# Performance work log

Measured on AMD Instinct MI355X. Metric: run time of the kernel, lower is better.

The kernel has to match this reference:

```python
import jax, jax.numpy as jnp
import numpy as np

BS, M, CLIP_DIM = 64, 1000, 512
D = 512
N_WAYS = 20
N_Z = 8


def setup_inputs() -> dict:
    key = jax.random.key(0)
    ks = jax.random.split(key, 16)
    s = 0.02
    inp = {
        "x_context": jax.random.normal(ks[0], (BS, M, CLIP_DIM), jnp.float32),
        "y_context": jax.random.randint(ks[1], (BS, M), 0, N_WAYS),
        "x_query": jax.random.normal(ks[2], (BS, M, CLIP_DIM), jnp.float32),
        # image_proj
        "Wp": jax.random.normal(ks[3], (CLIP_DIM, D), jnp.float32) * s,
        "bp": jnp.zeros((D,), jnp.float32),
        # aggregator: Linear(d,d) -> GELU -> Linear(d,2d)
        "Wa1": jax.random.normal(ks[4], (D, D), jnp.float32) * s,
        "ba1": jnp.zeros((D,), jnp.float32),
        "Wa2": jax.random.normal(ks[5], (D, 2 * D), jnp.float32) * s,
        "ba2": jnp.zeros((2 * D,), jnp.float32),
        # decoder: Linear(d,d) -> GELU -> Linear(d,d)
        "Wd1": jax.random.normal(ks[6], (D, D), jnp.float32) * s,
        "bd1": jnp.zeros((D,), jnp.float32),
        "Wd2": jax.random.normal(ks[7], (D, D), jnp.float32) * s,
        "bd2": jnp.zeros((D,), jnp.float32),
    }
    return inp


def reference(x_context, y_context, x_query, Wp, bp, Wa1, ba1, Wa2, ba2, Wd1, bd1, Wd2, bd2):
    # project image embeddings: [bs, M, clip_dim] -> [bs, M, d]
    xc = x_context @ Wp + bp
    xq = x_query @ Wp + bp

    # encode_context_per_class: per-class masked sum == one-hot segment-sum
    # (original loops over classes doing (x*mask).sum(dim=1))
    oh = jax.nn.one_hot(y_context, N_WAYS, dtype=xc.dtype)  # [bs, M, N]
    r_C = jnp.einsum('bmn,bmd->bnd', oh, xc)  # [bs, N, d]

    # knowledge is None -> k = zeros; combined = relu(r + 0)
    combined = jax.nn.relu(r_C)
    h = jax.nn.gelu(combined @ Wa1 + ba1, approximate=False)
    stats = h @ Wa2 + ba2  # [bs, N, 2d]
    mu, scale_raw = stats[..., :D], stats[..., D:]
    scale = 0.01 + 0.99 * jax.nn.softplus(scale_raw)

    # eval path: sample n_z from q(z|C) via reparameterization
    eps = jax.random.normal(jax.random.key(42), (N_Z,) + mu.shape, mu.dtype)
    z_samples = mu[None] + scale[None] * eps  # [n_z, bs, N, d]

    # decode: class weight vectors then inner product with queries
    W = jax.nn.gelu(z_samples @ Wd1 + bd1, approximate=False) @ Wd2 + bd2
    logits = jnp.einsum('bqd,sbnd->sbqn', xq, W)  # [n_z, bs, Q*N, N]
    return logits, z_samples, mu, scale
```

## Files before the change

### kernel.cpp

```cpp
#include <hip/hip_runtime.h>
#include <hip/hip_bf16.h>
#include <stdint.h>


typedef __attribute__((ext_vector_type(8))) short short8;
typedef __attribute__((ext_vector_type(4))) float f32x4;

__device__ __forceinline__ float gelu_f(float x) {
    return 0.5f * x * (1.0f + erff(x * 0.70710678118654752440f));
}
__device__ __forceinline__ float softplus_f(float x) {
    return fmaxf(x, 0.0f) + log1pf(expf(-fabsf(x)));
}
__device__ __forceinline__ uint32_t cvt2(float a, float b) {
    __hip_bfloat162 h;
    h.x = __float2bfloat16(a);
    h.y = __float2bfloat16(b);
    uint32_t u; __builtin_memcpy(&u, &h, 4); return u;
}
__device__ __forceinline__ unsigned short f2bfu(float f) {
    __hip_bfloat16 h = __float2bfloat16(f);
    unsigned short u; __builtin_memcpy(&u, &h, 2); return u;
}
__device__ __forceinline__ float bfu2f(unsigned short u) {
    uint32_t v = (uint32_t)u << 16; float f; __builtin_memcpy(&f, &v, 4); return f;
}

__device__ __forceinline__ void threefry2x32(uint32_t k0, uint32_t k1,
                                             uint32_t x0, uint32_t x1,
                                             uint32_t& o0, uint32_t& o1) {
    uint32_t ks[3] = {k0, k1, k0 ^ k1 ^ 0x1BD11BDAu};
    x0 += ks[0]; x1 += ks[1];
    const uint32_t rot[8] = {13,15,26,6,17,29,16,24};
#pragma unroll
    for (int i = 0; i < 5; i++) {
#pragma unroll
        for (int j = 0; j < 4; j++) {
            uint32_t r = rot[(i & 1) * 4 + j];
            x0 += x1;
            x1 = (x1 << r) | (x1 >> (32 - r));
            x1 ^= x0;
        }
        x0 += ks[(i + 1) % 3];
        x1 += ks[(i + 2) % 3] + (uint32_t)(i + 1);
    }
    o0 = x0; o1 = x1;
}

__device__ __forceinline__ float bits_to_normal(uint32_t b) {
    float f = __uint_as_float((b >> 9) | 0x3F800000u) - 1.0f;
    const float lo = __uint_as_float(0xBF7FFFFFu);
    float u = fmaxf(lo, f * 2.0f + lo);
    return 1.41421356237309504880f * erfinvf(u);
}

__global__ __launch_bounds__(256) void prep_k(
    const float* __restrict__ Wp, const float* __restrict__ Wa1,
    const float* __restrict__ Wa2, const float* __restrict__ Wd1,
    const float* __restrict__ Wd2, const float* __restrict__ bp,
    const float* __restrict__ bd2, const int* __restrict__ y,
    unsigned short* __restrict__ WpTb, unsigned short* __restrict__ Wa1Tb,
    unsigned short* __restrict__ Wa2Tb, unsigned short* __restrict__ WdT1b,
    unsigned short* __restrict__ Gtb,
    float* __restrict__ bv, float* __restrict__ w2bp,
    float* __restrict__ c0, float* __restrict__ cnt)
{
    __shared__ __align__(16) char sm[24576];
    __shared__ int lc[32];
    __shared__ float ws4[4];
    const int f = blockIdx.x;
    const int tid = threadIdx.x;

    if (f < 320) {
        float (*T)[65] = reinterpret_cast<float(*)[65]>(sm);
        const float* src; unsigned short* dst; int C, t, xb, yb;
        if (f < 64)       { src = Wp;  dst = WpTb;  C = 512;  t = f;       xb = t & 7;  yb = t >> 3; }
        else if (f < 128) { src = Wa1; dst = Wa1Tb; C = 512;  t = f - 64;  xb = t & 7;  yb = t >> 3; }
        else if (f < 256) { src = Wa2; dst = Wa2Tb; C = 1024; t = f - 128; xb = t & 15; yb = t >> 4; }
        else              { src = Wd1; dst = WdT1b; C = 512;  t = f - 256; xb = t & 7;  yb = t >> 3; }
        const int r0 = yb * 64, cc0 = xb * 64;
        const int rr = tid >> 4, cc = (tid & 15) * 4;
#pragma unroll
        for (int l = 0; l < 4; l++) {
            int row = rr + l * 16;
            float4 v = *(const float4*)&src[(size_t)(r0 + row) * C + cc0 + cc];
            T[row][cc] = v.x; T[row][cc+1] = v.y; T[row][cc+2] = v.z; T[row][cc+3] = v.w;
        }
        __syncthreads();
#pragma unroll
        for (int l = 0; l < 4; l++) {
            int n = rr + l * 16;
            uint2 u;
            u.x = cvt2(T[cc][n], T[cc+1][n]);
            u.y = cvt2(T[cc+2][n], T[cc+3][n]);
            *(uint2*)&dst[(size_t)(cc0 + n) * 512 + r0 + cc] = u;
        }
    } else if (f < 576) {
        const float* W = (f < 448) ? Wp : Wd2;
        const float* v = (f < 448) ? bd2 : bp;
        float* o = (f < 448) ? bv : w2bp;
        int t = (f < 448) ? f - 320 : f - 448;
        int wave = tid >> 6, lane = tid & 63;
        int r = t * 4 + wave;
        const float* row = W + (size_t)r * 512 + lane * 8;
        float4 x0 = *(const float4*)row;
        float4 x1 = *(const float4*)(row + 4);
        float4 v0 = *(const float4*)&v[lane * 8];
        float4 v1 = *(const float4*)&v[lane * 8 + 4];
        float s = x0.x*v0.x + x0.y*v0.y + x0.z*v0.z + x0.w*v0.w
                + x1.x*v1.x + x1.y*v1.y + x1.z*v1.z + x1.w*v1.w;
#pragma unroll
        for (int off = 32; off > 0; off >>= 1) s += __shfl_down(s, off, 64);
        if (lane == 0) o[r] = s;
    } else if (f == 576) {
        float s = bp[tid] * bd2[tid] + bp[tid + 256] * bd2[tid + 256];
#pragma unroll
        for (int off = 32; off > 0; off >>= 1) s += __shfl_down(s, off, 64);
        int wave = tid >> 6, lane = tid & 63;
        if (lane == 0) ws4[wave] = s;
        __syncthreads();
        if (tid == 0) c0[0] = ws4[0] + ws4[1] + ws4[2] + ws4[3];
    } else if (f < 641) {
        int b = f - 577;
        if (tid < 32) lc[tid] = 0;
        __syncthreads();
        for (int m = tid; m < 1000; m += 256)
            atomicAdd(&lc[y[b * 1000 + m]], 1);
        __syncthreads();
        if (tid < 20) cnt[b * 20 + tid] = (float)lc[tid];
    } else {
        unsigned short* As = (unsigned short*)sm;
        unsigned short* Bs = (unsigned short*)(sm + 8192);
        const int g = f - 641;
        const int lane = tid & 63, w = tid >> 6;
        const int row0 = (g >> 2) * 64, col0 = (g & 3) * 128;
        f32x4 acc[4][2] = {};
        for (int k0 = 0; k0 < 512; k0 += 64) {
            {
                int row = tid >> 2, cs = (tid & 3) * 16;
                int swz = (row & 7) << 4;
                const float* src = Wp + (size_t)(row0 + row) * 512 + k0 + cs;
#pragma unroll
                for (int j = 0; j < 2; j++) {
                    float4 v0 = *(const float4*)(src + j * 8);
                    float4 v1 = *(const float4*)(src + j * 8 + 4);
                    uint4 u;
                    u.x = cvt2(v0.x, v0.y); u.y = cvt2(v0.z, v0.w);
                    u.z = cvt2(v1.x, v1.y); u.w = cvt2(v1.z, v1.w);
                    *(uint4*)((char*)As + row * 128 + (((cs + j * 8) * 2) ^ swz)) = u;
                }
            }
            {
                int row = tid >> 1, cs = (tid & 1) * 32;
                int swz = (row & 7) << 4;
                const float* src = Wd2 + (size_t)(col0 + row) * 512 + k0 + cs;
#pragma unroll
                for (int j = 0; j < 4; j++) {
                    float4 v0 = *(const float4*)(src + j * 8);
                    float4 v1 = *(const float4*)(src + j * 8 + 4);
                    uint4 u;
                    u.x = cvt2(v0.x, v0.y); u.y = cvt2(v0.z, v0.w);
                    u.z = cvt2(v1.x, v1.y); u.w = cvt2(v1.z, v1.w);
                    *(uint4*)((char*)Bs + row * 128 + (((cs + j * 8) * 2) ^ swz)) = u;
                }
            }
            __syncthreads();
#pragma unroll
            for (int ks = 0; ks < 2; ks++) {
                short8 a[4], bb[2];
#pragma unroll
                for (int mi = 0; mi < 4; mi++) {
                    int r = mi * 16 + (lane & 15);
                    a[mi] = *(const short8*)((const char*)As + r * 128 +
                              (((ks * 32 + (lane >> 4) * 8) * 2) ^ ((r & 7) << 4)));
                }
#pragma unroll
                for (int ni = 0; ni < 2; ni++) {
                    int n = w * 32 + ni * 16 + (lane & 15);
                    bb[ni] = *(const short8*)((const char*)Bs + n * 128 +
                              (((ks * 32 + (lane >> 4) * 8) * 2) ^ ((n & 7) << 4)));
                }
#pragma unroll
                for (int mi = 0; mi < 4; mi++)
#pragma unroll
                    for (int ni = 0; ni < 2; ni++)
                        acc[mi][ni] = __builtin_amdgcn_mfma_f32_16x16x32_bf16(a[mi], bb[ni], acc[mi][ni], 0, 0, 0);
            }
            __syncthreads();
        }
#pragma unroll
        for (int mi = 0; mi < 4; mi++)
#pragma unroll
            for (int ni = 0; ni < 2; ni++) {
                int c = col0 + w * 32 + ni * 16 + (lane & 15);
#pragma unroll
                for (int j = 0; j < 4; j++) {
                    int r = row0 + mi * 16 + (lane >> 4) * 4 + j;
                    Gtb[(size_t)r * 512 + c] = f2bfu(acc[mi][ni][j]);
                }
            }
    }
}

__global__ __launch_bounds__(256) void onehot4_k(const float* __restrict__ xc,
                                                 const int* __restrict__ y,
                                                 float* __restrict__ Apart) {
    __shared__ unsigned short Xs[128 * 64];
    __shared__ int ys[256];
    const int chb = blockIdx.x * 128;
    const int mc = blockIdx.y;
    const int b = blockIdx.z;
    const int m00 = mc * 256;
    const int tid = threadIdx.x, lane = tid & 63, w = tid >> 6;
    const int chs = w * 32;

    {
        int mg = m00 + tid;
        ys[tid] = (mg < 1000) ? y[b * 1000 + mg] : -1;
    }

    f32x4 acc[2][2] = {};
    for (int step = 0; step < 4; step++) {
        const int k0 = step * 64;
        int m = m00 + k0 + lane; if (m > 999) m = 999;
        const float* src = xc + ((size_t)b * 1000 + m) * 512 + chb + chs;
        float x[32];
#pragma unroll
        for (int j8 = 0; j8 < 8; j8++) {
            float4 v = *(const float4*)(src + j8 * 4);
            x[j8*4+0]=v.x; x[j8*4+1]=v.y; x[j8*4+2]=v.z; x[j8*4+3]=v.w;
        }
        __syncthreads();
#pragma unroll
        for (int j = 0; j < 32; j++) {
            int ch = chs + j;
            *(unsigned short*)((char*)Xs + ch * 128 + ((lane * 2) ^ ((ch & 7) << 4)))
                = f2bfu(x[j]);
        }
        __syncthreads();
#pragma unroll
        for (int ks = 0; ks < 2; ks++) {
            int kb = ks * 32 + (lane >> 4) * 8;
            int4 yv0 = *(const int4*)&ys[k0 + kb];
            int4 yv1 = *(const int4*)&ys[k0 + kb + 4];
            int ya[8] = {yv0.x, yv0.y, yv0.z, yv0.w, yv1.x, yv1.y, yv1.z, yv1.w};
            short8 a[2];
#pragma unroll
            for (int mi = 0; mi < 2; mi++) {
                int cls = mi * 16 + (lane & 15);
#pragma unroll
                for (int e = 0; e < 8; e++)
                    a[mi][e] = (short)((ya[e] == cls) ? 0x3F80 : 0);
            }
            short8 bb[2];
#pragma unroll
            for (int ni = 0; ni < 2; ni++) {
                int ch = chs + ni * 16 + (lane & 15);
                bb[ni] = *(const short8*)((const char*)Xs + ch * 128 +
                           ((kb * 2) ^ ((ch & 7) << 4)));
            }
#pragma unroll
            for (int mi = 0; mi < 2; mi++)
#pragma unroll
                for (int ni = 0; ni < 2; ni++)
                    acc[mi][ni] = __builtin_amdgcn_mfma_f32_16x16x32_bf16(a[mi], bb[ni], acc[mi][ni], 0, 0, 0);
        }
    }
    float* dst = Apart + (size_t)mc * 655360;
#pragma unroll
    for (int mi = 0; mi < 2; mi++) {
#pragma unroll
        for (int ni = 0; ni < 2; ni++) {
            int ch = chb + chs + ni * 16 + (lane & 15);
#pragma unroll
            for (int j = 0; j < 4; j++) {
                int cls = mi * 16 + (lane >> 4) * 4 + j;
                if (cls < 20)
                    dst[((size_t)b * 20 + cls) * 512 + ch] = acc[mi][ni][j];
            }
        }
    }
}

template <int EPI, int MT, int A4>
__global__ __launch_bounds__(256) void gm2_k(const unsigned short* __restrict__ Abf,
                                             const unsigned short* __restrict__ Bbf,
                                             const float* __restrict__ bias,
                                             const float* __restrict__ extra,
                                             unsigned short* __restrict__ C0,
                                             float* __restrict__ F0,
                                             float* __restrict__ F1,
                                             int Nn) {
    __shared__ unsigned short As[MT * 64];
    __shared__ unsigned short Bs[128 * 64];
    const int tid = threadIdx.x;
    const int lane = tid & 63, w = tid >> 6;
    const int row0 = blockIdx.y * MT, col0 = blockIdx.x * 128;
    f32x4 acc[MT / 16][2] = {};
    for (int k0 = 0; k0 < 512; k0 += 64) {
        if constexpr (MT == 64) {
            int row = tid >> 2, cs = (tid & 3) * 16;
            int swz = (row & 7) << 4;
            const unsigned short* src = Abf + (size_t)(row0 + row) * 512 + k0 + cs;
#pragma unroll
            for (int j = 0; j < 2; j++) {
                uint4 u = *(const uint4*)(src + j * 8);
                *(uint4*)((char*)As + row * 128 + (((cs + j * 8) * 2) ^ swz)) = u;
            }
        } else {
            int row = tid >> 3, cs = (tid & 7) * 8;
            int swz = (row & 7) << 4;
            uint4 u;
            if constexpr (A4) {
                const float* p = (const float*)Abf + (size_t)(row0 + row) * 512 + k0 + cs;
                float4 s0 = *(const float4*)p;
                float4 s1 = *(const float4*)(p + 4);
#pragma unroll
                for (int q = 1; q < 4; q++) {
                    const float* pp = p + (size_t)q * 655360;
                    float4 v0 = *(const float4*)pp, v1 = *(const float4*)(pp + 4);
                    s0.x += v0.x; s0.y += v0.y; s0.z += v0.z; s0.w += v0.w;
                    s1.x += v1.x; s1.y += v1.y; s1.z += v1.z; s1.w += v1.w;
                }
                u.x = cvt2(s0.x, s0.y); u.y = cvt2(s0.z, s0.w);
                u.z = cvt2(s1.x, s1.y); u.w = cvt2(s1.z, s1.w);
            } else {
                u = *(const uint4*)(Abf + (size_t)(row0 + row) * 512 + k0 + cs);
            }
            *(uint4*)((char*)As + row * 128 + ((cs * 2) ^ swz)) = u;
        }
        {
            int row = tid >> 1, cs = (tid & 1) * 32;
            int swz = (row & 7) << 4;
            const unsigned short* src = Bbf + (size_t)(col0 + row) * 512 + k0 + cs;
#pragma unroll
            for (int j = 0; j < 4; j++) {
                uint4 u = *(const uint4*)(src + j * 8);
                *(uint4*)((char*)Bs + row * 128 + (((cs + j * 8) * 2) ^ swz)) = u;
            }
        }
        __syncthreads();
#pragma unroll
        for (int ks = 0; ks < 2; ks++) {
            short8 a[MT / 16], bb[2];
#pragma unroll
            for (int mi = 0; mi < MT / 16; mi++) {
                int r = mi * 16 + (lane & 15);
                a[mi] = *(const short8*)((const char*)As + r * 128 +
                          (((ks * 32 + (lane >> 4) * 8) * 2) ^ ((r & 7) << 4)));
            }
#pragma unroll
            for (int ni = 0; ni < 2; ni++) {
                int n = w * 32 + ni * 16 + (lane & 15);
                bb[ni] = *(const short8*)((const char*)Bs + n * 128 +
                          (((ks * 32 + (lane >> 4) * 8) * 2) ^ ((n & 7) << 4)));
            }
#pragma unroll
            for (int mi = 0; mi < MT / 16; mi++)
#pragma unroll
                for (int ni = 0; ni < 2; ni++)
                    acc[mi][ni] = __builtin_amdgcn_mfma_f32_16x16x32_bf16(a[mi], bb[ni], acc[mi][ni], 0, 0, 0);
        }
        __syncthreads();
    }
#pragma unroll
    for (int mi = 0; mi < MT / 16; mi++) {
#pragma unroll
        for (int ni = 0; ni < 2; ni++) {
            int c = col0 + w * 32 + ni * 16 + (lane & 15);
            float bvv = bias ? bias[c] : 0.f;
#pragma unroll
            for (int j = 0; j < 4; j++) {
                int r = row0 + mi * 16 + (lane >> 4) * 4 + j;
                float v = acc[mi][ni][j];
                if (EPI == 0) {
                    v += bvv;
                    C0[(size_t)r * Nn + c] = f2bfu(v);
                } else if (EPI == 1) {
                    v += extra[r] * bvv;
                    C0[(size_t)r * Nn + c] = f2bfu(fmaxf(v, 0.f));
                } else if (EPI == 2) {
                    C0[(size_t)r * Nn + c] = f2bfu(gelu_f(v + bvv));
                } else {
                    v += bvv;
                    if (c < 512) F0[(size_t)r * 512 + c] = v;
                    else F1[(size_t)r * 512 + (c - 512)] = 0.01f + 0.99f * softplus_f(v);
                }
            }
        }
    }
}

__global__ __launch_bounds__(256) void z2_k(const float* __restrict__ mu,
                                            const float* __restrict__ sc,
                                            float* __restrict__ z,
                                            unsigned short* __restrict__ zb) {
    const uint32_t NH = 2621440u;
    uint32_t i = blockIdx.x * 256u + threadIdx.x;
    if (i >= NH) return;
    uint32_t t0 = 2u * i;
    uint32_t o0, o1, p0, p1;
    threefry2x32(0u, 42u, 0u, t0, o0, o1);
    threefry2x32(0u, 42u, 0u, t0 + 1u, p0, p1);
    uint32_t r0 = t0 % 655360u;
    float2 mv = *(const float2*)&mu[r0];
    float2 sv = *(const float2*)&sc[r0];
    float z0 = mv.x + sv.x * bits_to_normal(o0 ^ o1);
    float z1 = mv.y + sv.y * bits_to_normal(p0 ^ p1);
    float2 zo; zo.x = z0; zo.y = z1;
    *(float2*)&z[t0] = zo;
    *(uint32_t*)&zb[t0] = cvt2(z0, z1);
}

__global__ __launch_bounds__(256) void beta2_k(const unsigned short* __restrict__ Wgb,
                                               const float* __restrict__ vec,
                                               const float* __restrict__ c0,
                                               float* __restrict__ beta) {
    int wave = threadIdx.x >> 6, lane = threadIdx.x & 63;
    int r = blockIdx.x * 4 + wave;
    short8 wv = *(const short8*)(Wgb + (size_t)r * 512 + lane * 8);
    float s = 0.f;
#pragma unroll
    for (int e = 0; e < 8; e++) s += vec[lane * 8 + e] * bfu2f((unsigned short)wv[e]);
#pragma unroll
    for (int o = 32; o > 0; o >>= 1) s += __shfl_down(s, o, 64);
    if (lane == 0) beta[r] = s + c0[0];
}

__global__ __launch_bounds__(512) void logits_mfma4_k(const float* __restrict__ Xq,
                                                      const unsigned short* __restrict__ Vb,
                                                      const float* __restrict__ beta,
                                                      float* __restrict__ out) {
    __shared__ unsigned short Vs[2][160 * 64];
    __shared__ float bs[160];
    const int u = blockIdx.x + 8 * blockIdx.y;
    const int xcd = u & 7, idx = u >> 3;
    const int b = (idx & 7) * 8 + xcd;
    const int qh = idx >> 3;
    const int tid = threadIdx.x, lane = tid & 63, w = tid >> 6;
    const int wq = w >> 1, wn = w & 1;

    if (tid < 160) {
        int s = tid / 20, n = tid - s * 20;
        bs[tid] = beta[(size_t)(s * 64 + b) * 20 + n];
    }

    auto stageV = [&](int buf, int k0) {
        for (int c = tid; c < 640; c += 512) {
            int row = c >> 2, off = (c & 3) * 32;
            int sdiv = row / 20;
            int row_g = row + sdiv * 1260 + b * 20;
            const unsigned short* src = Vb + (size_t)row_g * 512 + k0 + (c & 3) * 16;
            uint4 u0 = *(const uint4*)src;
            uint4 u1 = *(const uint4*)(src + 8);
            int swz = (row & 7) << 4;
            char* base = (char*)&Vs[buf][0] + row * 128;
            *(uint4*)(base + (off ^ swz)) = u0;
            *(uint4*)(base + ((off + 16) ^ swz)) = u1;
        }
    };

    const int klane = (lane >> 4) * 8;
    const float* xp[2];
    int qb[2];
#pragma unroll
    for (int qs = 0; qs < 2; qs++) {
        qb[qs] = qh * 128 + wq * 32 + qs * 16;
        int qr = qb[qs] + (lane & 15);
        if (qr > 999) qr = 999;
        xp[qs] = Xq + ((size_t)b * 1000 + qr) * 512 + klane;
    }
    int vrow[5], vswz[5];
#pragma unroll
    for (int nf = 0; nf < 5; nf++) {
        int rr = wn * 80 + nf * 16 + (lane & 15);
        vrow[nf] = rr * 128;
        vswz[nf] = (rr & 7) << 4;
    }

    stageV(0, 0);
    __syncthreads();

    f32x4 acc[2][5] = {};
    int cur = 0;
    for (int step = 0; step < 8; step++) {
        const int k0 = step * 64;
        if (step < 7) stageV(cur ^ 1, k0 + 64);
        const char* vbase = (const char*)&Vs[cur][0];
#pragma unroll
        for (int ks = 0; ks < 2; ks++) {
            int kb = (ks * 32 + klane) * 2;
            short8 bf[5];
#pragma unroll
            for (int nf = 0; nf < 5; nf++)
                bf[nf] = *(const short8*)(vbase + vrow[nf] + (kb ^ vswz[nf]));
            short8 af[2];
#pragma unroll
            for (int qs = 0; qs < 2; qs++) {
                const float* p = xp[qs] + k0 + ks * 32;
                float4 v0 = *(const float4*)p;
                float4 v1 = *(const float4*)(p + 4);
                uint4 uu;
                uu.x = cvt2(v0.x, v0.y); uu.y = cvt2(v0.z, v0.w);
                uu.z = cvt2(v1.x, v1.y); uu.w = cvt2(v1.z, v1.w);
                __builtin_memcpy(&af[qs], &uu, 16);
            }
#pragma unroll
            for (int qs = 0; qs < 2; qs++)
#pragma unroll
                for (int nf = 0; nf < 5; nf++)
                    acc[qs][nf] = __builtin_amdgcn_mfma_f32_16x16x32_bf16(af[qs], bf[nf], acc[qs][nf], 0, 0, 0);
        }
        __syncthreads();
        cur ^= 1;
    }

#pragma unroll
    for (int nf = 0; nf < 5; nf++) {
        int rl = wn * 80 + nf * 16 + (lane & 15);
        int s = rl / 20, n = rl - s * 20;
        float bb = bs[rl];
        size_t ob = (size_t)(s * 64 + b) * 20000;
#pragma unroll
        for (int qs = 0; qs < 2; qs++) {
#pragma unroll
            for (int j = 0; j < 4; j++) {
                int q = qb[qs] + (lane >> 4) * 4 + j;
                if (q < 1000)
                    out[ob + (size_t)q * 20 + n] = acc[qs][nf][j] + bb;
            }
        }
    }
}

extern "C" void kernel_launch(void* const* d_in, const int* in_sizes, int n_in,
                              void* d_out, int out_size, void* d_ws, size_t ws_size,
                              hipStream_t stream) {
    const float* x_context = (const float*)d_in[0];
    const int*   y_context = (const int*)d_in[1];
    const float* x_query   = (const float*)d_in[2];
    const float* Wp  = (const float*)d_in[3];
    const float* bp  = (const float*)d_in[4];
    const float* Wa1 = (const float*)d_in[5];
    const float* ba1 = (const float*)d_in[6];
    const float* Wa2 = (const float*)d_in[7];
    const float* ba2 = (const float*)d_in[8];
    const float* Wd1 = (const float*)d_in[9];
    const float* bd1 = (const float*)d_in[10];
    const float* Wd2 = (const float*)d_in[11];
    const float* bd2 = (const float*)d_in[12];

    float* out    = (float*)d_out;
    float* logits = out;
    float* z      = out + 10240000;
    float* mu     = out + 15482880;
    float* sc     = out + 16138240;

    float* ws   = (float*)d_ws;
    float* cnt  = ws;
    float* beta = cnt + 1280;
    float* bv   = beta + 10240;
    float* w2bp = bv + 512;
    float* c0   = w2bp + 512;
    unsigned short* WpTb  = (unsigned short*)(c0 + 63);
    unsigned short* Wa1Tb = WpTb + 262144;
    unsigned short* Wa2Tb = Wa1Tb + 262144;
    unsigned short* WdT1b = Wa2Tb + 524288;
    unsigned short* Gtb   = WdT1b + 262144;
    unsigned short* combb = Gtb + 262144;
    unsigned short* hb    = combb + 655360;
    unsigned short* zb    = hb + 655360;
    unsigned short* Vbf   = zb + 5242880;
    float* big = (float*)(Vbf + 5242880);
    unsigned short* Wgb = (unsigned short*)big;

    prep_k<<<dim3(673), 256, 0, stream>>>(Wp, Wa1, Wa2, Wd1, Wd2, bp, bd2, y_context,
                                          WpTb, Wa1Tb, Wa2Tb, WdT1b, Gtb,
                                          bv, w2bp, c0, cnt);
    onehot4_k<<<dim3(4, 4, 64), 256, 0, stream>>>(x_context, y_context, big);
    gm2_k<1, 32, 1><<<dim3(4, 40), 256, 0, stream>>>((const unsigned short*)big, WpTb, bp, cnt, combb, nullptr, nullptr, 512);
    gm2_k<2, 32, 0><<<dim3(4, 40), 256, 0, stream>>>(combb, Wa1Tb, ba1, nullptr, hb, nullptr, nullptr, 512);
    gm2_k<3, 32, 0><<<dim3(8, 40), 256, 0, stream>>>(hb, Wa2Tb, ba2, nullptr, nullptr, mu, sc, 1024);
    z2_k<<<dim3(10240), 256, 0, stream>>>(mu, sc, z, zb);
    gm2_k<2, 64, 0><<<dim3(4, 160), 256, 0, stream>>>(zb, WdT1b, bd1, nullptr, Wgb, nullptr, nullptr, 512);
    gm2_k<0, 64, 0><<<dim3(4, 160), 256, 0, stream>>>(Wgb, Gtb, bv, nullptr, Vbf, nullptr, nullptr, 512);
    beta2_k<<<dim3(2560), 256, 0, stream>>>(Wgb, w2bp, c0, beta);
    logits_mfma4_k<<<dim3(8, 64), 512, 0, stream>>>(x_query, Vbf, beta, logits);
}
```

Before: 224.2 us.

## Fuse onehot segment-sum into prep kernel and fuse decoder GEMMs with beta

The one-hot segment-sum blocks are appended to the weight-prep kernel as extra block indices, removing one launch. The two decoder GEMMs (z·Wd1 with GELU, then ·G) and the beta dot product become one kernel that keeps the 64x512 GELU intermediate in shared memory, so it is no longer written to or read back from global memory. The cost is that the fused kernel launches only 160 blocks of 512 threads with large shared memory, and its B operands come straight from global memory, so occupancy and parallelism drop compared with the earlier 640-block GEMMs.

```diff
diff --git a/kernel.cpp b/kernel.cpp
--- a/kernel.cpp
+++ b/kernel.cpp
@@ -54,19 +54,21 @@
     return 1.41421356237309504880f * erfinvf(u);
 }
 
-__global__ __launch_bounds__(256) void prep_k(
+__global__ __launch_bounds__(256) void po_k(
     const float* __restrict__ Wp, const float* __restrict__ Wa1,
     const float* __restrict__ Wa2, const float* __restrict__ Wd1,
     const float* __restrict__ Wd2, const float* __restrict__ bp,
     const float* __restrict__ bd2, const int* __restrict__ y,
+    const float* __restrict__ xc,
     unsigned short* __restrict__ WpTb, unsigned short* __restrict__ Wa1Tb,
     unsigned short* __restrict__ Wa2Tb, unsigned short* __restrict__ WdT1b,
     unsigned short* __restrict__ Gtb,
     float* __restrict__ bv, float* __restrict__ w2bp,
-    float* __restrict__ c0, float* __restrict__ cnt)
+    float* __restrict__ c0, float* __restrict__ cnt,
+    float* __restrict__ Apart)
 {
     __shared__ __align__(16) char sm[24576];
-    __shared__ int lc[32];
+    __shared__ int lc[256];
     __shared__ float ws4[4];
     const int f = blockIdx.x;
     const int tid = threadIdx.x;
@@ -128,7 +130,7 @@
             atomicAdd(&lc[y[b * 1000 + m]], 1);
         __syncthreads();
         if (tid < 20) cnt[b * 20 + tid] = (float)lc[tid];
-    } else {
+    } else if (f < 673) {
         unsigned short* As = (unsigned short*)sm;
         unsigned short* Bs = (unsigned short*)(sm + 8192);
         const int g = f - 641;
@@ -199,84 +201,79 @@
                     Gtb[(size_t)r * 512 + c] = f2bfu(acc[mi][ni][j]);
                 }
             }
-    }
-}
-
-__global__ __launch_bounds__(256) void onehot4_k(const float* __restrict__ xc,
-                                                 const int* __restrict__ y,
-                                                 float* __restrict__ Apart) {
-    __shared__ unsigned short Xs[128 * 64];
-    __shared__ int ys[256];
-    const int chb = blockIdx.x * 128;
-    const int mc = blockIdx.y;
-    const int b = blockIdx.z;
-    const int m00 = mc * 256;
-    const int tid = threadIdx.x, lane = tid & 63, w = tid >> 6;
-    const int chs = w * 32;
-
-    {
-        int mg = m00 + tid;
-        ys[tid] = (mg < 1000) ? y[b * 1000 + mg] : -1;
-    }
-
-    f32x4 acc[2][2] = {};
-    for (int step = 0; step < 4; step++) {
-        const int k0 = step * 64;
-        int m = m00 + k0 + lane; if (m > 999) m = 999;
-        const float* src = xc + ((size_t)b * 1000 + m) * 512 + chb + chs;
-        float x[32];
-#pragma unroll
-        for (int j8 = 0; j8 < 8; j8++) {
-            float4 v = *(const float4*)(src + j8 * 4);
-            x[j8*4+0]=v.x; x[j8*4+1]=v.y; x[j8*4+2]=v.z; x[j8*4+3]=v.w;
-        }
-        __syncthreads();
-#pragma unroll
-        for (int j = 0; j < 32; j++) {
-            int ch = chs + j;
-            *(unsigned short*)((char*)Xs + ch * 128 + ((lane * 2) ^ ((ch & 7) << 4)))
-                = f2bfu(x[j]);
-        }
-        __syncthreads();
-#pragma unroll
-        for (int ks = 0; ks < 2; ks++) {
-            int kb = ks * 32 + (lane >> 4) * 8;
-            int4 yv0 = *(const int4*)&ys[k0 + kb];
-            int4 yv1 = *(const int4*)&ys[k0 + kb + 4];
-            int ya[8] = {yv0.x, yv0.y, yv0.z, yv0.w, yv1.x, yv1.y, yv1.z, yv1.w};
-            short8 a[2];
-#pragma unroll
-            for (int mi = 0; mi < 2; mi++) {
-                int cls = mi * 16 + (lane & 15);
-#pragma unroll
-                for (int e = 0; e < 8; e++)
-                    a[mi][e] = (short)((ya[e] == cls) ? 0x3F80 : 0);
-            }
-            short8 bb[2];
+    } else {
+        unsigned short* Xs = (unsigned short*)sm;
+        int* ys = lc;
+        const int f2 = f - 673;
+        const int chb = (f2 & 3) * 128;
+        const int mc = (f2 >> 2) & 3;
+        const int b = f2 >> 4;
+        const int m00 = mc * 256;
+        const int lane = tid & 63, w = tid >> 6;
+        const int chs = w * 32;
+        {
+            int mg = m00 + tid;
+            ys[tid] = (mg < 1000) ? y[b * 1000 + mg] : -1;
+        }
+        f32x4 acc[2][2] = {};
+        for (int step = 0; step < 4; step++) {
+            const int k0 = step * 64;
+            int m = m00 + k0 + lane; if (m > 999) m = 999;
+            const float* src = xc + ((size_t)b * 1000 + m) * 512 + chb + chs;
+            float x[32];
+#pragma unroll
+            for (int j8 = 0; j8 < 8; j8++) {
+                float4 v = *(const float4*)(src + j8 * 4);
+                x[j8*4+0]=v.x; x[j8*4+1]=v.y; x[j8*4+2]=v.z; x[j8*4+3]=v.w;
+            }
+            __syncthreads();
+#pragma unroll
+            for (int j = 0; j < 32; j++) {
+                int ch = chs + j;
+                *(unsigned short*)((char*)Xs + ch * 128 + ((lane * 2) ^ ((ch & 7) << 4)))
+                    = f2bfu(x[j]);
+            }
+            __syncthreads();
+#pragma unroll
+            for (int ks = 0; ks < 2; ks++) {
+                int kb = ks * 32 + (lane >> 4) * 8;
+                int4 yv0 = *(const int4*)&ys[k0 + kb];
+                int4 yv1 = *(const int4*)&ys[k0 + kb + 4];
+                int ya[8] = {yv0.x, yv0.y, yv0.z, yv0.w, yv1.x, yv1.y, yv1.z, yv1.w};
+                short8 a[2];
+#pragma unroll
+                for (int mi = 0; mi < 2; mi++) {
+                    int cls = mi * 16 + (lane & 15);
+#pragma unroll
+                    for (int e = 0; e < 8; e++)
+                        a[mi][e] = (short)((ya[e] == cls) ? 0x3F80 : 0);
+                }
+                short8 bb[2];
+#pragma unroll
+                for (int ni = 0; ni < 2; ni++) {
+                    int ch = chs + ni * 16 + (lane & 15);
+                    bb[ni] = *(const short8*)((const char*)Xs + ch * 128 +
+                               ((kb * 2) ^ ((ch & 7) << 4)));
+                }
+#pragma unroll
+                for (int mi = 0; mi < 2; mi++)
+#pragma unroll
+                    for (int ni = 0; ni < 2; ni++)
+                        acc[mi][ni] = __builtin_amdgcn_mfma_f32_16x16x32_bf16(a[mi], bb[ni], acc[mi][ni], 0, 0, 0);
+            }
+        }
+        float* dst = Apart + (size_t)mc * 655360;
+#pragma unroll
+        for (int mi = 0; mi < 2; mi++) {
 #pragma unroll
             for (int ni = 0; ni < 2; ni++) {
-                int ch = chs + ni * 16 + (lane & 15);
-                bb[ni] = *(const short8*)((const char*)Xs + ch * 128 +
-                           ((kb * 2) ^ ((ch & 7) << 4)));
-            }
-#pragma unroll
-            for (int mi = 0; mi < 2; mi++)
-#pragma unroll
-                for (int ni = 0; ni < 2; ni++)
-                    acc[mi][ni] = __builtin_amdgcn_mfma_f32_16x16x32_bf16(a[mi], bb[ni], acc[mi][ni], 0, 0, 0);
-        }
-    }
-    float* dst = Apart + (size_t)mc * 655360;
-#pragma unroll
-    for (int mi = 0; mi < 2; mi++) {
-#pragma unroll
-        for (int ni = 0; ni < 2; ni++) {
-            int ch = chb + chs + ni * 16 + (lane & 15);
-#pragma unroll
-            for (int j = 0; j < 4; j++) {
-                int cls = mi * 16 + (lane >> 4) * 4 + j;
-                if (cls < 20)
-                    dst[((size_t)b * 20 + cls) * 512 + ch] = acc[mi][ni][j];
+                int ch = chb + chs + ni * 16 + (lane & 15);
+#pragma unroll
+                for (int j = 0; j < 4; j++) {
+                    int cls = mi * 16 + (lane >> 4) * 4 + j;
+                    if (cls < 20)
+                        dst[((size_t)b * 20 + cls) * 512 + ch] = acc[mi][ni][j];
+                }
             }
         }
     }
@@ -412,19 +409,122 @@
     *(uint32_t*)&zb[t0] = cvt2(z0, z1);
 }
 
-__global__ __launch_bounds__(256) void beta2_k(const unsigned short* __restrict__ Wgb,
-                                               const float* __restrict__ vec,
-                                               const float* __restrict__ c0,
-                                               float* __restrict__ beta) {
-    int wave = threadIdx.x >> 6, lane = threadIdx.x & 63;
-    int r = blockIdx.x * 4 + wave;
-    short8 wv = *(const short8*)(Wgb + (size_t)r * 512 + lane * 8);
-    float s = 0.f;
-#pragma unroll
-    for (int e = 0; e < 8; e++) s += vec[lane * 8 + e] * bfu2f((unsigned short)wv[e]);
-#pragma unroll
-    for (int o = 32; o > 0; o >>= 1) s += __shfl_down(s, o, 64);
-    if (lane == 0) beta[r] = s + c0[0];
+__global__ __launch_bounds__(512) void wgv_k(const unsigned short* __restrict__ zb,
+                                             const unsigned short* __restrict__ Wd1T,
+                                             const unsigned short* __restrict__ Gt,
+                                             const float* __restrict__ bd1,
+                                             const float* __restrict__ bv,
+                                             const float* __restrict__ w2bp,
+                                             const float* __restrict__ c0,
+                                             unsigned short* __restrict__ Vbf,
+                                             float* __restrict__ beta) {
+    __shared__ unsigned short Wg[64 * 512];
+    __shared__ unsigned short As[64 * 64];
+    const int r0 = blockIdx.x * 64;
+    const int tid = threadIdx.x, lane = tid & 63, w = tid >> 6;
+    const int col0 = w * 64;
+
+    f32x4 acc[4][4] = {};
+    for (int k0 = 0; k0 < 512; k0 += 64) {
+        {
+            int row = tid >> 3, cs = (tid & 7) * 8;
+            int swz = (row & 7) << 4;
+            uint4 u = *(const uint4*)(zb + (size_t)(r0 + row) * 512 + k0 + cs);
+            *(uint4*)((char*)As + row * 128 + ((cs * 2) ^ swz)) = u;
+        }
+        __syncthreads();
+#pragma unroll
+        for (int ks = 0; ks < 2; ks++) {
+            int kb = ks * 32 + (lane >> 4) * 8;
+            short8 a[4], bb[4];
+#pragma unroll
+            for (int mi = 0; mi < 4; mi++) {
+                int r = mi * 16 + (lane & 15);
+                a[mi] = *(const short8*)((const char*)As + r * 128 +
+                          ((kb * 2) ^ ((r & 7) << 4)));
+            }
+#pragma unroll
+            for (int ni = 0; ni < 4; ni++) {
+                int n = col0 + ni * 16 + (lane & 15);
+                bb[ni] = *(const short8*)(Wd1T + (size_t)n * 512 + k0 + kb);
+            }
+#pragma unroll
+            for (int mi = 0; mi < 4; mi++)
+#pragma unroll
+                for (int ni = 0; ni < 4; ni++)
+                    acc[mi][ni] = __builtin_amdgcn_mfma_f32_16x16x32_bf16(a[mi], bb[ni], acc[mi][ni], 0, 0, 0);
+        }
+        __syncthreads();
+    }
+#pragma unroll
+    for (int mi = 0; mi < 4; mi++) {
+#pragma unroll
+        for (int ni = 0; ni < 4; ni++) {
+            int c = col0 + ni * 16 + (lane & 15);
+            float bvv = bd1[c];
+#pragma unroll
+            for (int j = 0; j < 4; j++) {
+                int r = mi * 16 + (lane >> 4) * 4 + j;
+                float v = gelu_f(acc[mi][ni][j] + bvv);
+                *(unsigned short*)((char*)Wg + r * 1024 + ((c * 2) ^ ((r & 7) << 4)))
+                    = f2bfu(v);
+            }
+        }
+    }
+    __syncthreads();
+
+    {
+        int row = tid >> 3, p = tid & 7;
+        const char* base = (const char*)Wg + row * 1024;
+        int swz = (row & 7) << 4;
+        float s = 0.f;
+#pragma unroll
+        for (int j = 0; j < 64; j++) {
+            int c = p * 64 + j;
+            s += bfu2f(*(const unsigned short*)(base + ((c * 2) ^ swz))) * w2bp[c];
+        }
+#pragma unroll
+        for (int off = 4; off > 0; off >>= 1) s += __shfl_down(s, off, 64);
+        if (p == 0) beta[r0 + row] = s + c0[0];
+    }
+
+    f32x4 acc2[4][4] = {};
+    for (int k0 = 0; k0 < 512; k0 += 64) {
+#pragma unroll
+        for (int ks = 0; ks < 2; ks++) {
+            int kb = ks * 32 + (lane >> 4) * 8;
+            short8 a[4], bb[4];
+#pragma unroll
+            for (int mi = 0; mi < 4; mi++) {
+                int r = mi * 16 + (lane & 15);
+                a[mi] = *(const short8*)((const char*)Wg + r * 1024 +
+                          (((k0 + kb) * 2) ^ ((r & 7) << 4)));
+            }
+#pragma unroll
+            for (int ni = 0; ni < 4; ni++) {
+                int n = col0 + ni * 16 + (lane & 15);
+                bb[ni] = *(const short8*)(Gt + (size_t)n * 512 + k0 + kb);
+            }
+#pragma unroll
+            for (int mi = 0; mi < 4; mi++)
+#pragma unroll
+                for (int ni = 0; ni < 4; ni++)
+                    acc2[mi][ni] = __builtin_amdgcn_mfma_f32_16x16x32_bf16(a[mi], bb[ni], acc2[mi][ni], 0, 0, 0);
+        }
+    }
+#pragma unroll
+    for (int mi = 0; mi < 4; mi++) {
+#pragma unroll
+        for (int ni = 0; ni < 4; ni++) {
+            int c = col0 + ni * 16 + (lane & 15);
+            float bvv = bv[c];
+#pragma unroll
+            for (int j = 0; j < 4; j++) {
+                int r = r0 + mi * 16 + (lane >> 4) * 4 + j;
+                Vbf[(size_t)r * 512 + c] = f2bfu(acc2[mi][ni][j] + bvv);
+            }
+        }
+    }
 }
 
 __global__ __launch_bounds__(512) void logits_mfma4_k(const float* __restrict__ Xq,
@@ -572,18 +672,15 @@
     unsigned short* zb    = hb + 655360;
     unsigned short* Vbf   = zb + 5242880;
     float* big = (float*)(Vbf + 5242880);
-    unsigned short* Wgb = (unsigned short*)big;
-
-    prep_k<<<dim3(673), 256, 0, stream>>>(Wp, Wa1, Wa2, Wd1, Wd2, bp, bd2, y_context,
-                                          WpTb, Wa1Tb, Wa2Tb, WdT1b, Gtb,
-                                          bv, w2bp, c0, cnt);
-    onehot4_k<<<dim3(4, 4, 64), 256, 0, stream>>>(x_context, y_context, big);
+
+    po_k<<<dim3(1697), 256, 0, stream>>>(Wp, Wa1, Wa2, Wd1, Wd2, bp, bd2, y_context,
+                                         x_context,
+                                         WpTb, Wa1Tb, Wa2Tb, WdT1b, Gtb,
+                                         bv, w2bp, c0, cnt, big);
     gm2_k<1, 32, 1><<<dim3(4, 40), 256, 0, stream>>>((const unsigned short*)big, WpTb, bp, cnt, combb, nullptr, nullptr, 512);
     gm2_k<2, 32, 0><<<dim3(4, 40), 256, 0, stream>>>(combb, Wa1Tb, ba1, nullptr, hb, nullptr, nullptr, 512);
     gm2_k<3, 32, 0><<<dim3(8, 40), 256, 0, stream>>>(hb, Wa2Tb, ba2, nullptr, nullptr, mu, sc, 1024);
     z2_k<<<dim3(10240), 256, 0, stream>>>(mu, sc, z, zb);
-    gm2_k<2, 64, 0><<<dim3(4, 160), 256, 0, stream>>>(zb, WdT1b, bd1, nullptr, Wgb, nullptr, nullptr, 512);
-    gm2_k<0, 64, 0><<<dim3(4, 160), 256, 0, stream>>>(Wgb, Gtb, bv, nullptr, Vbf, nullptr, nullptr, 512);
-    beta2_k<<<dim3(2560), 256, 0, stream>>>(Wgb, w2bp, c0, beta);
+    wgv_k<<<dim3(160), 512, 0, stream>>>(zb, WdT1b, Gtb, bd1, bv, w2bp, c0, Vbf, beta);
     logits_mfma4_k<<<dim3(8, 64), 512, 0, stream>>>(x_query, Vbf, beta, logits);
 }
```

Result: faster. 216.1 us (median of 2 runs) (-3.6%).
